# Optimization experiments

Measured on AMD Instinct MI355X. Metric: run time of the kernel, lower is better.

## Reference

```python
import jax, jax.numpy as jnp
import numpy as np

N = 50000          # nodes per node type
F = 256            # input feature dim
C = 256            # hidden_channels
H, D = 8, 32       # heads, head_dim (C = H*D)
E = 200000         # edges per edge type
OUT = 16           # out_channels
SRC = (0, 1, 0)    # edge type -> source node-type index (user,item)
DST = (1, 0, 0)    # edge type -> destination node-type index
LABELED = 1        # labeled_class = 'item'


def setup_inputs() -> dict:
    key = jax.random.key(0)
    ks = jax.random.split(key, 24)
    s = 0.06  # ~1/sqrt(256) init scale
    inp = {
        'x': jax.random.normal(ks[0], (2, N, F), jnp.float32),
        'edge_index': jax.random.randint(ks[1], (3, 2, E), 0, N, jnp.int64),
        'lin_w': jax.random.normal(ks[2], (2, F, C), jnp.float32) * s,
        'lin_b': jnp.zeros((2, C), jnp.float32),
        'k_w': jax.random.normal(ks[3], (2, C, C), jnp.float32) * s,
        'k_b': jnp.zeros((2, C), jnp.float32),
        'q_w': jax.random.normal(ks[4], (2, C, C), jnp.float32) * s,
        'q_b': jnp.zeros((2, C), jnp.float32),
        'v_w': jax.random.normal(ks[5], (2, C, C), jnp.float32) * s,
        'v_b': jnp.zeros((2, C), jnp.float32),
        'a_w': jax.random.normal(ks[6], (2, C, C), jnp.float32) * s,
        'a_b': jnp.zeros((2, C), jnp.float32),
        'skip': jnp.ones((2,), jnp.float32),
        'a_rel': jax.random.normal(ks[7], (3, H, D, D), jnp.float32) * (1.0 / np.sqrt(D)),
        'm_rel': jax.random.normal(ks[8], (3, H, D, D), jnp.float32) * (1.0 / np.sqrt(D)),
        'p_rel': jnp.ones((3, H), jnp.float32),
        'out_w': jax.random.normal(ks[9], (C, OUT), jnp.float32) * s,
        'out_b': jnp.zeros((OUT,), jnp.float32),
    }
    return inp


def _segment_softmax(alpha, idx, n):
    # alpha: [E, H], idx: [E] destination node ids
    amax = jax.ops.segment_max(alpha, idx, num_segments=n)
    amax = jnp.where(jnp.isfinite(amax), amax, 0.0)
    ex = jnp.exp(alpha - amax[idx])
    den = jax.ops.segment_sum(ex, idx, num_segments=n)
    return ex / (den[idx] + 1e-16)


def reference(x, edge_index, lin_w, lin_b, k_w, k_b, q_w, q_b, v_w, v_b,
              a_w, a_b, skip, a_rel, m_rel, p_rel, out_w, out_b):
    # per-node-type input Linear + ReLU
    h = jax.nn.relu(jnp.einsum('tnf,tfc->tnc', x, lin_w) + lin_b[:, None, :])

    def proj(w, b):
        return (jnp.einsum('tnc,tce->tne', h, w) + b[:, None, :]).reshape(2, N, H, D)

    k = proj(k_w, k_b)
    q = proj(q_w, q_b)
    v = proj(v_w, v_b)

    agg = jnp.zeros((2, N, H, D), h.dtype)
    for t in range(3):  # fixed small loop over edge types
        s, d = SRC[t], DST[t]
        src_idx, dst_idx = edge_index[t, 0], edge_index[t, 1]
        # relation-specific transforms of source keys / values
        k_rel = jnp.einsum('nhd,hde->nhe', k[s], a_rel[t])
        v_rel = jnp.einsum('nhd,hde->nhe', v[s], m_rel[t])
        # per-edge attention logits [E, H]
        alpha = (q[d][dst_idx] * k_rel[src_idx]).sum(-1) * p_rel[t] / (D ** 0.5)
        alpha = _segment_softmax(alpha, dst_idx, N)
        msg = v_rel[src_idx] * alpha[..., None]          # [E, H, D]
        agg = agg.at[d].add(jax.ops.segment_sum(msg, dst_idx, num_segments=N))

    o = agg.reshape(2, N, C)
    o = jnp.einsum('tnc,tce->tne', jax.nn.gelu(o, approximate=False), a_w) + a_b[:, None, :]
    beta = jax.nn.sigmoid(skip)[:, None, None]
    o = beta * o + (1.0 - beta) * h                      # skip connection (in == out dims)

    return o[LABELED] @ out_w + out_b                    # logits for labeled_class='item'
```

## Files before the change

kernel.cpp:

```cpp
#include <hip/hip_runtime.h>
#include <hip/hip_bf16.h>

using u16 = unsigned short;
using u32 = unsigned int;

#define NNODES 50000
#define NEDGE  200000
#define DEGCAP 64
#define NT     3125

__device__ __forceinline__ float blo2f(u32 u) { u32 v = u << 16; float f; __builtin_memcpy(&f, &v, 4); return f; }
__device__ __forceinline__ float bhi2f(u32 u) { u32 v = u & 0xffff0000u; float f; __builtin_memcpy(&f, &v, 4); return f; }
__device__ __forceinline__ float b2f(u16 u) { u32 v = ((u32)u) << 16; float f; __builtin_memcpy(&f, &v, 4); return f; }
__device__ __forceinline__ u16 f2b(float f) {
  __hip_bfloat16 h = __float2bfloat16(f);
  u16 r; __builtin_memcpy(&r, &h, 2); return r;
}
__device__ __forceinline__ float gelu_exact(float x) {
  return 0.5f * x * (1.f + erff(x * 0.70710678118654752f));
}

__device__ __forceinline__ void gload16(const void* gp, void* lp) {
  __builtin_amdgcn_global_load_lds(
      (__attribute__((address_space(1))) u32*)(const_cast<void*>(gp)),
      (__attribute__((address_space(3))) u32*)lp, 16, 0, 0);
}

__device__ __forceinline__ void wait_vm0() {
  asm volatile("s_waitcnt vmcnt(0)" ::: "memory");
}
__device__ __forceinline__ void wait_vm2() {
  asm volatile("s_waitcnt vmcnt(2)" ::: "memory");
}

typedef __bf16 bh8 __attribute__((ext_vector_type(8)));
typedef float f32x4 __attribute__((ext_vector_type(4)));

struct GArg { const u16* A; const u16* B; const float* bias; u16* C; };

__device__ __forceinline__ void stage_tile(const u16* At, u16* buf, int lane) {
#pragma unroll
  for (int i = 0; i < 8; ++i) {
    const int row = i * 2 + (lane >> 5);
    const int c   = (lane & 31) ^ (row & 7);
    gload16(At + (size_t)row * 256 + c * 8, buf + i * 512 + lane * 8);
  }
}

__device__ __forceinline__ void stage_tile_blk(const u16* At, u16* buf, int wave, int lane) {
#pragma unroll
  for (int i = 0; i < 2; ++i) {
    const int row = wave * 4 + i * 2 + (lane >> 5);
    const int c   = (lane & 31) ^ (row & 7);
    gload16(At + (size_t)row * 256 + c * 8, buf + wave * 1024 + i * 512 + lane * 8);
  }
}

template <int MODE>
__launch_bounds__(256, 2)
__global__ void gemm_v8(GArg g0, GArg g1, GArg g2)
{
  GArg ga = (blockIdx.z == 0) ? g0 : ((blockIdx.z == 1) ? g1 : g2);
  const int tid  = threadIdx.x;
  const int lane = tid & 63;
  const int wave = tid >> 6;
  const int lr = lane & 15;
  const int lq = lane >> 4;
  const int colbase = wave * 64;

  __shared__ alignas(16) u16 lds[2][4096];
  __shared__ alignas(16) u16 pat[4][1152];
  u16* wl = &pat[wave][0];

  bh8 B[4][8];
#pragma unroll
  for (int s = 0; s < 4; ++s) {
    const u16* bp = ga.B + (size_t)(colbase + s * 16 + lr) * 256 + lq * 8;
#pragma unroll
    for (int ks = 0; ks < 8; ++ks) B[s][ks] = *(const bh8*)(bp + ks * 32);
  }
  float bias[4];
#pragma unroll
  for (int s = 0; s < 4; ++s) bias[s] = ga.bias[colbase + s * 16 + lr];

  int foff[8];
#pragma unroll
  for (int ks = 0; ks < 8; ++ks)
    foff[ks] = lr * 256 + (((ks * 4 + lq) ^ (lr & 7)) * 8);

  const int t0 = blockIdx.x;
  const int ts = gridDim.x;

  stage_tile_blk(ga.A + (size_t)t0 * 4096, &lds[0][0], wave, lane);
  int cur = 0;

  for (int t = t0; t < NT; t += ts) {
    const int tn = t + ts;
    if (tn < NT)
      stage_tile_blk(ga.A + (size_t)tn * 4096, &lds[cur ^ 1][0], wave, lane);
    wait_vm2();
    __builtin_amdgcn_s_barrier();

    const u16* buf = &lds[cur][0];
    bh8 ab[8];
#pragma unroll
    for (int ks = 0; ks < 8; ++ks) ab[ks] = *(const bh8*)(buf + foff[ks]);

    f32x4 acc[4];
#pragma unroll
    for (int s = 0; s < 4; ++s) acc[s] = (f32x4){0.f, 0.f, 0.f, 0.f};
#pragma unroll
    for (int ks = 0; ks < 8; ++ks) {
#pragma unroll
      for (int s = 0; s < 4; ++s)
        acc[s] = __builtin_amdgcn_mfma_f32_16x16x32_bf16(ab[ks], B[s][ks], acc[s], 0, 0, 0);
    }

#pragma unroll
    for (int s = 0; s < 4; ++s) {
#pragma unroll
      for (int r = 0; r < 4; ++r) {
        float v = acc[s][r] + bias[s];
        if (MODE == 0) v = fmaxf(v, 0.f);
        wl[(lq * 4 + r) * 72 + s * 16 + lr] = f2b(v);
      }
    }
#pragma unroll
    for (int j = 0; j < 2; ++j) {
      const int row = (lane >> 3) + j * 8;
      const int seg = lane & 7;
      const uint4 pv = *(const uint4*)(wl + row * 72 + seg * 8);
      *(uint4*)(ga.C + ((size_t)t * 16 + row) * 256 + colbase + seg * 8) = pv;
    }
    __builtin_amdgcn_s_barrier();
    cur ^= 1;
  }
}

__global__ void cvt_x_k(const float* __restrict__ x, u16* __restrict__ xb) {
  const int id = blockIdx.x * 256 + threadIdx.x;
  if (id >= (2 * NNODES * 256) / 8) return;
  const float4 a = ((const float4*)x)[id * 2];
  const float4 b = ((const float4*)x)[id * 2 + 1];
  uint4 o;
  o.x = (u32)f2b(a.x) | ((u32)f2b(a.y) << 16);
  o.y = (u32)f2b(a.z) | ((u32)f2b(a.w) << 16);
  o.z = (u32)f2b(b.x) | ((u32)f2b(b.y) << 16);
  o.w = (u32)f2b(b.z) | ((u32)f2b(b.w) << 16);
  ((uint4*)xb)[id] = o;
}

__global__ void prep_w_k(const float* __restrict__ lin_w, const float* __restrict__ q_w,
                         const float* __restrict__ a_w, const float* __restrict__ k_w,
                         const float* __restrict__ v_w, const float* __restrict__ k_b,
                         const float* __restrict__ v_b, const float* __restrict__ a_rel,
                         const float* __restrict__ m_rel, const float* __restrict__ out_w,
                         const float* __restrict__ a_b, const float* __restrict__ out_b,
                         const float* __restrict__ skipv,
                         u16* __restrict__ lin0T, u16* __restrict__ lin1T,
                         u16* __restrict__ qT,
                         u16* __restrict__ kfT, u16* __restrict__ vfT,
                         u16* __restrict__ WcT, float* __restrict__ bfin,
                         float* __restrict__ bkf, float* __restrict__ bvf)
{
  const int tid = blockIdx.x * 256 + threadIdx.x;
  const int nn = tid >> 8, kk = tid & 255;
  switch (blockIdx.y) {
    case 0: lin0T[tid] = f2b(lin_w[kk * 256 + nn]); break;
    case 1: lin1T[tid] = f2b(lin_w[65536 + kk * 256 + nn]); break;
    case 2: qT[tid] = f2b(q_w[65536 + kk * 256 + nn]); break;
    case 3: {
      const int h = nn >> 5, e = nn & 31;
      float s = 0.f;
      for (int d = 0; d < 32; ++d) s += k_w[kk * 256 + h * 32 + d] * a_rel[(h * 32 + d) * 32 + e];
      kfT[tid] = f2b(s);
      if (kk == 0) {
        float sb = 0.f;
        for (int d = 0; d < 32; ++d) sb += k_b[h * 32 + d] * a_rel[(h * 32 + d) * 32 + e];
        bkf[nn] = sb;
      }
      break;
    }
    case 4: {
      const int h = nn >> 5, e = nn & 31;
      float s = 0.f;
      for (int d = 0; d < 32; ++d) s += v_w[kk * 256 + h * 32 + d] * m_rel[(h * 32 + d) * 32 + e];
      vfT[tid] = f2b(s);
      if (kk == 0) {
        float sb = 0.f;
        for (int d = 0; d < 32; ++d) sb += v_b[h * 32 + d] * m_rel[(h * 32 + d) * 32 + e];
        bvf[nn] = sb;
      }
      break;
    }
    default: {
      const float beta = 1.f / (1.f + __expf(-skipv[1]));
      if (tid < 8192) {
        const int j = tid & 15;
        const int k = tid >> 4;
        float s;
        if (k < 256) {
          float acc = 0.f;
          for (int d = 0; d < 256; ++d)
            acc += a_w[65536 + k * 256 + d] * out_w[d * 16 + j];
          s = beta * acc;
        } else {
          s = (1.f - beta) * out_w[(k - 256) * 16 + j];
        }
        WcT[j * 512 + k] = f2b(s);
      }
      if (tid < 16) {
        float acc = 0.f;
        for (int c = 0; c < 256; ++c) acc += a_b[256 + c] * out_w[c * 16 + tid];
        bfin[tid] = beta * acc + out_b[tid];
      }
      break;
    }
  }
}

__global__ void scatter_k(const int* __restrict__ ei, int* __restrict__ cnt, int* __restrict__ srcl) {
  const int e = blockIdx.x * 256 + threadIdx.x;
  if (e >= NEDGE) return;
  const int src = ei[e];
  const int dst = ei[NEDGE + e];
  if ((unsigned)dst >= NNODES || (unsigned)src >= NNODES) return;
  const int pos = atomicAdd(&cnt[dst], 1);
  if (pos < DEGCAP) srcl[(size_t)dst * DEGCAP + pos] = src;
}

__global__ void edge_agg_k(const u16* __restrict__ qb, const u16* __restrict__ krel,
                           const u16* __restrict__ vrel, const int* __restrict__ cnt,
                           const int* __restrict__ srcl, const float* __restrict__ prel,
                           u16* __restrict__ g)
{
  const int node = (blockIdx.x * blockDim.x + threadIdx.x) >> 6;
  if (node >= NNODES) return;
  const int lane = threadIdx.x & 63;
  const int hh = lane >> 3;
  const int off = hh * 32 + (lane & 7) * 4;
  const float scale = prel[hh] * 0.17677669529663687f;
  const uint2 qv = *(const uint2*)(qb + (size_t)node * 256 + off);
  const float q0 = blo2f(qv.x) * scale, q1 = bhi2f(qv.x) * scale;
  const float q2 = blo2f(qv.y) * scale, q3 = bhi2f(qv.y) * scale;
  int dg = cnt[node]; if (dg > DEGCAP) dg = DEGCAP;
  const int* sl = srcl + (size_t)node * DEGCAP;
  float den = 0.f, a0 = 0.f, a1 = 0.f, a2 = 0.f, a3 = 0.f;
  for (int i = 0; i < dg; ++i) {
    const int src = sl[i];
    const uint2 kv = *(const uint2*)(krel + (size_t)src * 256 + off);
    float p = q0 * blo2f(kv.x) + q1 * bhi2f(kv.x) + q2 * blo2f(kv.y) + q3 * bhi2f(kv.y);
    p += __shfl_xor(p, 1);
    p += __shfl_xor(p, 2);
    p += __shfl_xor(p, 4);
    const float ex = __expf(p);
    const uint2 vv = *(const uint2*)(vrel + (size_t)src * 256 + off);
    den += ex;
    a0 += ex * blo2f(vv.x); a1 += ex * bhi2f(vv.x);
    a2 += ex * blo2f(vv.y); a3 += ex * bhi2f(vv.y);
  }
  float r0 = 0.f, r1 = 0.f, r2 = 0.f, r3 = 0.f;
  if (dg > 0) {
    const float inv = 1.f / den;
    r0 = gelu_exact(a0 * inv); r1 = gelu_exact(a1 * inv);
    r2 = gelu_exact(a2 * inv); r3 = gelu_exact(a3 * inv);
  }
  uint2 gv;
  gv.x = (u32)f2b(r0) | ((u32)f2b(r1) << 16);
  gv.y = (u32)f2b(r2) | ((u32)f2b(r3) << 16);
  *(uint2*)(g + (size_t)node * 256 + off) = gv;
}

__launch_bounds__(256, 2)
__global__ void final_k(const u16* __restrict__ g, const u16* __restrict__ h1,
                        const u16* __restrict__ WcT, const float* __restrict__ bfin,
                        float* __restrict__ out)
{
  const int tid = threadIdx.x;
  const int lane = tid & 63;
  const int wave = tid >> 6;
  const int lr = lane & 15;
  const int lq = lane >> 4;

  __shared__ alignas(16) u16 lds[4][8192];
  u16* buf = &lds[wave][0];

  bh8 B[16];
  {
    const u16* bp = WcT + (size_t)lr * 512 + lq * 8;
#pragma unroll
    for (int ks = 0; ks < 16; ++ks) B[ks] = *(const bh8*)(bp + ks * 32);
  }
  const float bv = bfin[lr];

  int foff[8];
#pragma unroll
  for (int ks = 0; ks < 8; ++ks)
    foff[ks] = lr * 256 + (((ks * 4 + lq) ^ (lr & 7)) * 8);

  const int wt0 = blockIdx.x * 4 + wave;
  const int wts = gridDim.x * 4;

  for (int t = wt0; t < NT; t += wts) {
    stage_tile(g  + (size_t)t * 4096, buf,        lane);
    stage_tile(h1 + (size_t)t * 4096, buf + 4096, lane);
    wait_vm0();
    f32x4 acc = {0.f, 0.f, 0.f, 0.f};
#pragma unroll
    for (int ks = 0; ks < 8; ++ks)
      acc = __builtin_amdgcn_mfma_f32_16x16x32_bf16(*(const bh8*)(buf + foff[ks]), B[ks], acc, 0, 0, 0);
#pragma unroll
    for (int ks = 0; ks < 8; ++ks)
      acc = __builtin_amdgcn_mfma_f32_16x16x32_bf16(*(const bh8*)(buf + 4096 + foff[ks]), B[ks + 8], acc, 0, 0, 0);
#pragma unroll
    for (int r = 0; r < 4; ++r)
      out[((size_t)t * 16 + lq * 4 + r) * 16 + lr] = acc[r] + bv;
  }
}

extern "C" void kernel_launch(void* const* d_in, const int* in_sizes, int n_in,
                              void* d_out, int out_size, void* d_ws, size_t ws_size,
                              hipStream_t stream)
{
  const float* x     = (const float*)d_in[0];
  const int*   ei    = (const int*)d_in[1];
  const float* lin_w = (const float*)d_in[2];
  const float* lin_b = (const float*)d_in[3];
  const float* k_w   = (const float*)d_in[4];
  const float* k_b   = (const float*)d_in[5];
  const float* q_w   = (const float*)d_in[6];
  const float* q_b   = (const float*)d_in[7];
  const float* v_w   = (const float*)d_in[8];
  const float* v_b   = (const float*)d_in[9];
  const float* a_w   = (const float*)d_in[10];
  const float* a_b   = (const float*)d_in[11];
  const float* skipv = (const float*)d_in[12];
  const float* a_rel = (const float*)d_in[13];
  const float* m_rel = (const float*)d_in[14];
  const float* p_rel = (const float*)d_in[15];
  const float* out_w = (const float*)d_in[16];
  const float* out_b = (const float*)d_in[17];
  char* ws = (char*)d_ws;

  u16*  xb    = (u16*)(ws + 0);
  u16*  h0    = (u16*)(ws + 51200000);
  u16*  h1    = (u16*)(ws + 76800000);
  u16*  qb    = (u16*)(ws + 102400000);
  u16*  gbuf  = (u16*)(ws + 128000000);
  u16*  krel  = (u16*)(ws + 0);
  u16*  vrel  = (u16*)(ws + 25600000);
  char* W     = ws + 153600000;
  u16*  lin0T = (u16*)(W + 0);
  u16*  lin1T = (u16*)(W + 131072);
  u16*  qT    = (u16*)(W + 2 * 131072);
  u16*  kfT   = (u16*)(W + 3 * 131072);
  u16*  vfT   = (u16*)(W + 4 * 131072);
  u16*  WcT   = (u16*)(W + 5 * 131072);
  float* bfin = (float*)(W + 5 * 131072 + 16384);
  float* bkf  = (float*)(W + 5 * 131072 + 17408);
  float* bvf  = (float*)(W + 5 * 131072 + 18432);
  int*  cnt   = (int*)(W + 5 * 131072 + 19456);
  int*  srcl  = (int*)(W + 5 * 131072 + 19456 + 200000);

  hipMemsetAsync(cnt, 0, NNODES * sizeof(int), stream);
  prep_w_k<<<dim3(256, 6), 256, 0, stream>>>(lin_w, q_w, a_w, k_w, v_w, k_b, v_b,
                                             a_rel, m_rel, out_w, a_b, out_b, skipv,
                                             lin0T, lin1T, qT, kfT, vfT, WcT, bfin, bkf, bvf);
  scatter_k<<<(NEDGE + 255) / 256, 256, 0, stream>>>(ei, cnt, srcl);
  cvt_x_k<<<12500, 256, 0, stream>>>(x, xb);

  {
    GArg a0{xb, lin0T, lin_b, h0};
    GArg a1{xb + (size_t)NNODES * 256, lin1T, lin_b + 256, h1};
    gemm_v8<0><<<dim3(256, 1, 2), 256, 0, stream>>>(a0, a1, a0);
  }
  {
    GArg a0{h1, qT, q_b + 256, qb};
    GArg a1{h0, kfT, bkf, krel};
    GArg a2{h0, vfT, bvf, vrel};
    gemm_v8<1><<<dim3(170, 1, 3), 256, 0, stream>>>(a0, a1, a2);
  }
  edge_agg_k<<<12500, 256, 0, stream>>>(qb, krel, vrel, cnt, srcl, p_rel, gbuf);
  final_k<<<512, 256, 0, stream>>>(gbuf, h1, WcT, bfin, (float*)d_out);
}
```

Baseline: 346.6 us.

## Fuse fp32-to-bf16 input conversion into first GEMM and prefetch edge gathers

Removes the separate x conversion kernel: the first GEMM now stages fp32 tiles of x directly into LDS and converts them to bf16 in registers before the MFMA. This avoids writing and re-reading a 51MB bf16 copy of x, at the cost of doubling LDS per stage and adding conversion work. The cnt memset is folded into the weight-prep kernel as an extra grid row, saving one launch. The edge aggregation loop now loads the source list once per lane, broadcasts it with shuffles, and software-prefetches the next edge's K/V rows.

```diff
diff --git a/kernel.cpp b/kernel.cpp
--- a/kernel.cpp
+++ b/kernel.cpp
@@ -11,7 +11,6 @@
 
 __device__ __forceinline__ float blo2f(u32 u) { u32 v = u << 16; float f; __builtin_memcpy(&f, &v, 4); return f; }
 __device__ __forceinline__ float bhi2f(u32 u) { u32 v = u & 0xffff0000u; float f; __builtin_memcpy(&f, &v, 4); return f; }
-__device__ __forceinline__ float b2f(u16 u) { u32 v = ((u32)u) << 16; float f; __builtin_memcpy(&f, &v, 4); return f; }
 __device__ __forceinline__ u16 f2b(float f) {
   __hip_bfloat16 h = __float2bfloat16(f);
   u16 r; __builtin_memcpy(&r, &h, 2); return r;
@@ -26,12 +25,9 @@
       (__attribute__((address_space(3))) u32*)lp, 16, 0, 0);
 }
 
-__device__ __forceinline__ void wait_vm0() {
-  asm volatile("s_waitcnt vmcnt(0)" ::: "memory");
-}
-__device__ __forceinline__ void wait_vm2() {
-  asm volatile("s_waitcnt vmcnt(2)" ::: "memory");
-}
+__device__ __forceinline__ void wait_vm0() { asm volatile("s_waitcnt vmcnt(0)" ::: "memory"); }
+__device__ __forceinline__ void wait_vm2() { asm volatile("s_waitcnt vmcnt(2)" ::: "memory"); }
+__device__ __forceinline__ void wait_vm4() { asm volatile("s_waitcnt vmcnt(4)" ::: "memory"); }
 
 typedef __bf16 bh8 __attribute__((ext_vector_type(8)));
 typedef float f32x4 __attribute__((ext_vector_type(4)));
@@ -47,7 +43,7 @@
   }
 }
 
-__device__ __forceinline__ void stage_tile_blk(const u16* At, u16* buf, int wave, int lane) {
+__device__ __forceinline__ void stage_blk_bf16(const u16* At, u16* buf, int wave, int lane) {
 #pragma unroll
   for (int i = 0; i < 2; ++i) {
     const int row = wave * 4 + i * 2 + (lane >> 5);
@@ -56,9 +52,18 @@
   }
 }
 
-template <int MODE>
+__device__ __forceinline__ void stage_blk_f32(const float* At, float* buf, int wave, int lane) {
+#pragma unroll
+  for (int i = 0; i < 4; ++i) {
+    const int row = wave * 4 + i;
+    const int c   = lane ^ ((row & 7) << 1);
+    gload16(At + (size_t)row * 256 + c * 4, buf + row * 256 + lane * 4);
+  }
+}
+
+template <int MODE, bool F32A>
 __launch_bounds__(256, 2)
-__global__ void gemm_v8(GArg g0, GArg g1, GArg g2)
+__global__ void gemm_v9(GArg g0, GArg g1, GArg g2)
 {
   GArg ga = (blockIdx.z == 0) ? g0 : ((blockIdx.z == 1) ? g1 : g2);
   const int tid  = threadIdx.x;
@@ -68,7 +73,8 @@
   const int lq = lane >> 4;
   const int colbase = wave * 64;
 
-  __shared__ alignas(16) u16 lds[2][4096];
+  constexpr int TW = F32A ? 8192 : 4096;
+  __shared__ alignas(16) u16 lds[2][TW];
   __shared__ alignas(16) u16 pat[4][1152];
   u16* wl = &pat[wave][0];
 
@@ -85,26 +91,45 @@
 
   int foff[8];
 #pragma unroll
-  for (int ks = 0; ks < 8; ++ks)
-    foff[ks] = lr * 256 + (((ks * 4 + lq) ^ (lr & 7)) * 8);
+  for (int ks = 0; ks < 8; ++ks) {
+    if (F32A)
+      foff[ks] = lr * 256 + (((ks * 8 + lq * 2) ^ ((lr & 7) << 1)) * 4);
+    else
+      foff[ks] = lr * 256 + (((ks * 4 + lq) ^ (lr & 7)) * 8);
+  }
 
   const int t0 = blockIdx.x;
   const int ts = gridDim.x;
 
-  stage_tile_blk(ga.A + (size_t)t0 * 4096, &lds[0][0], wave, lane);
+  if (F32A) stage_blk_f32((const float*)ga.A + (size_t)t0 * 4096, (float*)&lds[0][0], wave, lane);
+  else      stage_blk_bf16(ga.A + (size_t)t0 * 4096, &lds[0][0], wave, lane);
   int cur = 0;
 
   for (int t = t0; t < NT; t += ts) {
     const int tn = t + ts;
-    if (tn < NT)
-      stage_tile_blk(ga.A + (size_t)tn * 4096, &lds[cur ^ 1][0], wave, lane);
-    wait_vm2();
+    if (tn < NT) {
+      if (F32A) { stage_blk_f32((const float*)ga.A + (size_t)tn * 4096, (float*)&lds[cur ^ 1][0], wave, lane); wait_vm4(); }
+      else      { stage_blk_bf16(ga.A + (size_t)tn * 4096, &lds[cur ^ 1][0], wave, lane); wait_vm2(); }
+    } else {
+      wait_vm0();
+    }
     __builtin_amdgcn_s_barrier();
 
-    const u16* buf = &lds[cur][0];
     bh8 ab[8];
-#pragma unroll
-    for (int ks = 0; ks < 8; ++ks) ab[ks] = *(const bh8*)(buf + foff[ks]);
+    if (F32A) {
+      const float* fbuf = (const float*)&lds[cur][0];
+#pragma unroll
+      for (int ks = 0; ks < 8; ++ks) {
+        const f32x4 lo = *(const f32x4*)(fbuf + foff[ks]);
+        const f32x4 hi = *(const f32x4*)(fbuf + foff[ks] + 4);
+#pragma unroll
+        for (int j = 0; j < 4; ++j) { ab[ks][j] = (__bf16)lo[j]; ab[ks][j + 4] = (__bf16)hi[j]; }
+      }
+    } else {
+      const u16* buf = &lds[cur][0];
+#pragma unroll
+      for (int ks = 0; ks < 8; ++ks) ab[ks] = *(const bh8*)(buf + foff[ks]);
+    }
 
     f32x4 acc[4];
 #pragma unroll
@@ -135,19 +160,6 @@
     __builtin_amdgcn_s_barrier();
     cur ^= 1;
   }
-}
-
-__global__ void cvt_x_k(const float* __restrict__ x, u16* __restrict__ xb) {
-  const int id = blockIdx.x * 256 + threadIdx.x;
-  if (id >= (2 * NNODES * 256) / 8) return;
-  const float4 a = ((const float4*)x)[id * 2];
-  const float4 b = ((const float4*)x)[id * 2 + 1];
-  uint4 o;
-  o.x = (u32)f2b(a.x) | ((u32)f2b(a.y) << 16);
-  o.y = (u32)f2b(a.z) | ((u32)f2b(a.w) << 16);
-  o.z = (u32)f2b(b.x) | ((u32)f2b(b.y) << 16);
-  o.w = (u32)f2b(b.z) | ((u32)f2b(b.w) << 16);
-  ((uint4*)xb)[id] = o;
 }
 
 __global__ void prep_w_k(const float* __restrict__ lin_w, const float* __restrict__ q_w,
@@ -161,7 +173,8 @@
                          u16* __restrict__ qT,
                          u16* __restrict__ kfT, u16* __restrict__ vfT,
                          u16* __restrict__ WcT, float* __restrict__ bfin,
-                         float* __restrict__ bkf, float* __restrict__ bvf)
+                         float* __restrict__ bkf, float* __restrict__ bvf,
+                         int* __restrict__ cnt)
 {
   const int tid = blockIdx.x * 256 + threadIdx.x;
   const int nn = tid >> 8, kk = tid & 255;
@@ -193,7 +206,7 @@
       }
       break;
     }
-    default: {
+    case 5: {
       const float beta = 1.f / (1.f + __expf(-skipv[1]));
       if (tid < 8192) {
         const int j = tid & 15;
@@ -216,6 +229,9 @@
       }
       break;
     }
+    default:
+      if (tid < NNODES) cnt[tid] = 0;
+      break;
   }
 }
 
@@ -244,20 +260,31 @@
   const float q0 = blo2f(qv.x) * scale, q1 = bhi2f(qv.x) * scale;
   const float q2 = blo2f(qv.y) * scale, q3 = bhi2f(qv.y) * scale;
   int dg = cnt[node]; if (dg > DEGCAP) dg = DEGCAP;
-  const int* sl = srcl + (size_t)node * DEGCAP;
+  const int mysrc = srcl[(size_t)node * DEGCAP + lane];
+
   float den = 0.f, a0 = 0.f, a1 = 0.f, a2 = 0.f, a3 = 0.f;
+  uint2 kv = {0, 0}, vv = {0, 0};
+  if (dg > 0) {
+    const int s0 = __shfl(mysrc, 0);
+    kv = *(const uint2*)(krel + (size_t)s0 * 256 + off);
+    vv = *(const uint2*)(vrel + (size_t)s0 * 256 + off);
+  }
   for (int i = 0; i < dg; ++i) {
-    const int src = sl[i];
-    const uint2 kv = *(const uint2*)(krel + (size_t)src * 256 + off);
+    uint2 kn = kv, vn = vv;
+    if (i + 1 < dg) {
+      const int sn = __shfl(mysrc, i + 1);
+      kn = *(const uint2*)(krel + (size_t)sn * 256 + off);
+      vn = *(const uint2*)(vrel + (size_t)sn * 256 + off);
+    }
     float p = q0 * blo2f(kv.x) + q1 * bhi2f(kv.x) + q2 * blo2f(kv.y) + q3 * bhi2f(kv.y);
     p += __shfl_xor(p, 1);
     p += __shfl_xor(p, 2);
     p += __shfl_xor(p, 4);
     const float ex = __expf(p);
-    const uint2 vv = *(const uint2*)(vrel + (size_t)src * 256 + off);
     den += ex;
     a0 += ex * blo2f(vv.x); a1 += ex * bhi2f(vv.x);
     a2 += ex * blo2f(vv.y); a3 += ex * bhi2f(vv.y);
+    kv = kn; vv = vn;
   }
   float r0 = 0.f, r1 = 0.f, r2 = 0.f, r3 = 0.f;
   if (dg > 0) {
@@ -342,13 +369,12 @@
   const float* out_b = (const float*)d_in[17];
   char* ws = (char*)d_ws;
 
-  u16*  xb    = (u16*)(ws + 0);
-  u16*  h0    = (u16*)(ws + 51200000);
-  u16*  h1    = (u16*)(ws + 76800000);
-  u16*  qb    = (u16*)(ws + 102400000);
+  u16*  h0    = (u16*)(ws + 0);
+  u16*  h1    = (u16*)(ws + 25600000);
+  u16*  qb    = (u16*)(ws + 51200000);
+  u16*  krel  = (u16*)(ws + 76800000);
+  u16*  vrel  = (u16*)(ws + 102400000);
   u16*  gbuf  = (u16*)(ws + 128000000);
-  u16*  krel  = (u16*)(ws + 0);
-  u16*  vrel  = (u16*)(ws + 25600000);
   char* W     = ws + 153600000;
   u16*  lin0T = (u16*)(W + 0);
   u16*  lin1T = (u16*)(W + 131072);
@@ -362,23 +388,22 @@
   int*  cnt   = (int*)(W + 5 * 131072 + 19456);
   int*  srcl  = (int*)(W + 5 * 131072 + 19456 + 200000);
 
-  hipMemsetAsync(cnt, 0, NNODES * sizeof(int), stream);
-  prep_w_k<<<dim3(256, 6), 256, 0, stream>>>(lin_w, q_w, a_w, k_w, v_w, k_b, v_b,
+  prep_w_k<<<dim3(256, 7), 256, 0, stream>>>(lin_w, q_w, a_w, k_w, v_w, k_b, v_b,
                                              a_rel, m_rel, out_w, a_b, out_b, skipv,
-                                             lin0T, lin1T, qT, kfT, vfT, WcT, bfin, bkf, bvf);
+                                             lin0T, lin1T, qT, kfT, vfT, WcT, bfin,
+                                             bkf, bvf, cnt);
   scatter_k<<<(NEDGE + 255) / 256, 256, 0, stream>>>(ei, cnt, srcl);
-  cvt_x_k<<<12500, 256, 0, stream>>>(x, xb);
 
   {
-    GArg a0{xb, lin0T, lin_b, h0};
-    GArg a1{xb + (size_t)NNODES * 256, lin1T, lin_b + 256, h1};
-    gemm_v8<0><<<dim3(256, 1, 2), 256, 0, stream>>>(a0, a1, a0);
+    GArg a0{(const u16*)x, lin0T, lin_b, h0};
+    GArg a1{(const u16*)(x + (size_t)NNODES * 256), lin1T, lin_b + 256, h1};
+    gemm_v9<0, true><<<dim3(256, 1, 2), 256, 0, stream>>>(a0, a1, a0);
   }
   {
     GArg a0{h1, qT, q_b + 256, qb};
     GArg a1{h0, kfT, bkf, krel};
     GArg a2{h0, vfT, bvf, vrel};
-    gemm_v8<1><<<dim3(170, 1, 3), 256, 0, stream>>>(a0, a1, a2);
+    gemm_v9<1, false><<<dim3(170, 1, 3), 256, 0, stream>>>(a0, a1, a2);
   }
   edge_agg_k<<<12500, 256, 0, stream>>>(qb, krel, vrel, cnt, srcl, p_rel, gbuf);
   final_k<<<512, 256, 0, stream>>>(gbuf, h1, WcT, bfin, (float*)d_out);
```

Result: faster. 324.2 us (-6.5%).
